# Optimization experiments

Hardware: AMD Instinct MI355X
Metric: run time of the kernel (lower is better)

The kernel has to match this reference:

```python
import jax, jax.numpy as jnp
import numpy as np

B, T, C, H = 2, 2048, 1024, 16
D = C // H  # head dim 64


def setup_inputs() -> dict:
    key = jax.random.key(0)
    k1, k2, k3, k4, k5 = jax.random.split(key, 5)
    s = 0.02
    return {
        "x": jax.random.normal(k1, (B, T, C), jnp.float32),
        "w_attn": jax.random.normal(k2, (C, 3 * C), jnp.float32) * s,
        "b_attn": jnp.zeros((3 * C,), jnp.float32),
        "w_proj": jax.random.normal(k3, (C, C), jnp.float32) * s,
        "b_proj": jnp.zeros((C,), jnp.float32),
    }


def reference(x, w_attn, b_attn, w_proj, b_proj):
    b, t, c = x.shape
    qkv = x @ w_attn + b_attn  # [B,T,3C]
    q, k, v = jnp.split(qkv, 3, axis=-1)
    # [B,T,C] -> [B,H,T,D]
    q = q.reshape(b, t, H, D).transpose(0, 2, 1, 3)
    k = k.reshape(b, t, H, D).transpose(0, 2, 1, 3)
    v = v.reshape(b, t, H, D).transpose(0, 2, 1, 3)
    scores = jnp.einsum("bhqd,bhkd->bhqk", q, k) * (1.0 / jnp.sqrt(jnp.float32(D)))
    causal = jnp.tril(jnp.ones((t, t), bool))
    scores = jnp.where(causal[None, None], scores, jnp.float32(-jnp.inf))
    attn = jax.nn.softmax(scores, axis=-1)
    out = jnp.einsum("bhqk,bhkd->bhqd", attn, v)  # [B,H,T,D]
    out = out.transpose(0, 2, 1, 3).reshape(b, t, c)
    return out @ w_proj + b_proj
```

## Files before the change

kernel.cpp:

```cpp
#include <hip/hip_runtime.h>
#include <hip/hip_bf16.h>

#define B_ 2
#define T_ 2048
#define C_ 1024
#define H_ 16
#define D_ 64
#define M1 4096
#define N1 3072
#define K_ 1024

typedef __attribute__((ext_vector_type(8))) __bf16 bf16x8;
typedef __attribute__((ext_vector_type(4))) float f32x4;
typedef __attribute__((ext_vector_type(8))) unsigned short ushort8_t;
typedef __attribute__((ext_vector_type(4))) unsigned short ushort4_t;
typedef __attribute__((ext_vector_type(2))) unsigned int uint2_t;

static __device__ __forceinline__ unsigned short f2bf(float f) {
    unsigned int u = __builtin_bit_cast(unsigned int, f);
    u += 0x7fffu + ((u >> 16) & 1u);
    return (unsigned short)(u >> 16);
}
static __device__ __forceinline__ unsigned short f2bf_hw(float f) {
    return __builtin_bit_cast(unsigned short, (__bf16)f);
}
static __device__ __forceinline__ unsigned int packbf(float lo, float hi) {
    return (unsigned int)f2bf_hw(lo) | ((unsigned int)f2bf_hw(hi) << 16);
}
static __device__ __forceinline__ bf16x8 bload(const unsigned short* p) {
    return __builtin_bit_cast(bf16x8, *(const ushort8_t*)p);
}

#if defined(__has_builtin)
#if __has_builtin(__builtin_amdgcn_exp2f)
#define HAVE_EXP2_BUILTIN 1
#endif
#endif
static __device__ __forceinline__ float fexp2(float x) {
#ifdef HAVE_EXP2_BUILTIN
    return __builtin_amdgcn_exp2f(x);
#else
    float r; asm("v_exp_f32 %0, %1" : "=v"(r) : "v"(x)); return r;
#endif
}

typedef __attribute__((address_space(1))) const unsigned int gu32;
typedef __attribute__((address_space(3))) unsigned int lu32;
static __device__ __forceinline__ void gld16(const void* g, void* l) {
    __builtin_amdgcn_global_load_lds((gu32*)g, (lu32*)l, 16, 0, 0);
}

#define VMCNT(n) asm volatile("s_waitcnt vmcnt(" #n ")" ::: "memory")
#define LGKM0    asm volatile("s_waitcnt lgkmcnt(0)" ::: "memory")

__global__ void cast_x_kernel(const float* __restrict__ in,
                              unsigned short* __restrict__ out, int n4) {
    int idx = blockIdx.x * blockDim.x + threadIdx.x;
    int stride = gridDim.x * blockDim.x;
    for (int i = idx; i < n4; i += stride) {
        float4 v = ((const float4*)in)[i];
        ushort4_t o;
        o.x = f2bf(v.x); o.y = f2bf(v.y); o.z = f2bf(v.z); o.w = f2bf(v.w);
        ((ushort4_t*)out)[i] = o;
    }
}

__global__ void transpose_cast_kernel(const float* __restrict__ in,
                                      unsigned short* __restrict__ out,
                                      int K, int N) {
    __shared__ float tile[32][33];
    int tx = threadIdx.x & 31;
    int ty = threadIdx.x >> 5;
    int n0 = blockIdx.x * 32;
    int k0 = blockIdx.y * 32;
#pragma unroll
    for (int rr = 0; rr < 32; rr += 8)
        tile[ty + rr][tx] = in[(size_t)(k0 + ty + rr) * N + n0 + tx];
    __syncthreads();
#pragma unroll
    for (int rr = 0; rr < 32; rr += 8)
        out[(size_t)(n0 + ty + rr) * K + k0 + tx] = f2bf(tile[tx][ty + rr]);
}

template <bool SWAP>
static __device__ __forceinline__ void gemm_loop(
    const unsigned short* __restrict__ A, const unsigned short* __restrict__ Bt,
    unsigned short (*As)[128 * 32], unsigned short (*Bs)[128 * 32],
    int row0, int col0, int tid, f32x4 (&acc)[4][4])
{
    const int lane = tid & 63;
    const int wave = tid >> 6;
    const int g = lane >> 4, cl = lane & 15;
    const int wr = (wave >> 1) * 64, wc = (wave & 1) * 64;
    const int srow = tid >> 2;
    const int sgran = tid & 3;
#pragma unroll
    for (int m = 0; m < 4; ++m)
#pragma unroll
        for (int n = 0; n < 4; ++n)
            acc[m][n] = (f32x4){0.f, 0.f, 0.f, 0.f};
    auto stage = [&](int buf, int k0) {
#pragma unroll
        for (int c = 0; c < 2; ++c) {
            int r = srow + c * 64;
            int lg = sgran ^ ((r >> 1) & 3);
            gld16(A + (size_t)(row0 + r) * K_ + k0 + lg * 8,
                  (char*)&As[buf][0] + c * 4096 + wave * 1024);
            gld16(Bt + (size_t)(col0 + r) * K_ + k0 + lg * 8,
                  (char*)&Bs[buf][0] + c * 4096 + wave * 1024);
        }
    };
    stage(0, 0);
    int buf = 0;
    for (int k0 = 0; k0 < K_; k0 += 32) {
        if (k0 + 32 < K_) { stage(buf ^ 1, k0 + 32); VMCNT(4); }
        else              { VMCNT(0); }
        __builtin_amdgcn_s_barrier();
        bf16x8 af[4], bfv[4];
#pragma unroll
        for (int m = 0; m < 4; ++m) {
            int ra = wr + m * 16 + cl;
            af[m] = bload(&As[buf][ra * 32 + (g ^ ((ra >> 1) & 3)) * 8]);
        }
#pragma unroll
        for (int n = 0; n < 4; ++n) {
            int rb = wc + n * 16 + cl;
            bfv[n] = bload(&Bs[buf][rb * 32 + (g ^ ((rb >> 1) & 3)) * 8]);
        }
#pragma unroll
        for (int m = 0; m < 4; ++m)
#pragma unroll
            for (int n = 0; n < 4; ++n)
                acc[m][n] = SWAP
                    ? __builtin_amdgcn_mfma_f32_16x16x32_bf16(bfv[n], af[m], acc[m][n], 0, 0, 0)
                    : __builtin_amdgcn_mfma_f32_16x16x32_bf16(af[m], bfv[n], acc[m][n], 0, 0, 0);
        LGKM0;
        __builtin_amdgcn_s_barrier();
        buf ^= 1;
    }
}

__global__ __launch_bounds__(256)
void gemm_qkv_kernel(const unsigned short* __restrict__ A,
                     const unsigned short* __restrict__ Bt,
                     const float* __restrict__ bias,
                     unsigned short* __restrict__ Qo,
                     unsigned short* __restrict__ Ko,
                     unsigned short* __restrict__ Vt)
{
    __shared__ unsigned short As[2][128 * 32];
    __shared__ unsigned short Bs[2][128 * 32];
    const int lin = blockIdx.x + gridDim.x * blockIdx.y;
    const int xcd = lin & 7;
    const int idx = lin >> 3;
    const int bx = (xcd >> 1) * 8 + (idx & 7);
    const int by = (xcd & 1) * 12 + (idx >> 3);
    const int row0 = bx * 128, col0 = by * 128;

    const int tid = threadIdx.x;
    const int lane = tid & 63;
    const int wave = tid >> 6;
    const int g = lane >> 4, cl = lane & 15;
    const int wr = (wave >> 1) * 64, wc = (wave & 1) * 64;
    const float QSCALE = 0.125f * 1.44269504088896340736f;

    f32x4 acc[4][4];
    if (by >= 16) {
        gemm_loop<false>(A, Bt, As, Bs, row0, col0, tid, acc);
#pragma unroll
        for (int m = 0; m < 4; ++m) {
            int i0 = row0 + wr + m * 16 + g * 4;
            int b = i0 >> 11, t0 = i0 & 2047;
#pragma unroll
            for (int n = 0; n < 4; ++n) {
                int j = col0 + wc + n * 16 + cl;
                int c = j & 1023;
                int h = c >> 6, d = c & 63;
                float bv = bias[j];
                size_t bh = (size_t)(b * H_ + h);
                uint2_t w;
                w.x = packbf(acc[m][n][0] + bv, acc[m][n][1] + bv);
                w.y = packbf(acc[m][n][2] + bv, acc[m][n][3] + bv);
                *(uint2_t*)&Vt[(bh * D_ + d) * T_ + t0] = w;
            }
        }
    } else {
        gemm_loop<true>(A, Bt, As, Bs, row0, col0, tid, acc);
        const int jbase = col0 + wc;
        const int which = jbase >> 10;
        const int h = (jbase & 1023) >> 6;
        unsigned short* dst = which ? Ko : Qo;
        const float s = which ? 1.0f : QSCALE;
#pragma unroll
        for (int m = 0; m < 4; ++m) {
            int i = row0 + wr + m * 16 + cl;
            int b = i >> 11, t = i & 2047;
            size_t bh = (size_t)(b * H_ + h);
#pragma unroll
            for (int n = 0; n < 4; ++n) {
                int d0 = n * 16 + g * 4;
                float4 bv = *(const float4*)&bias[jbase + d0];
                uint2_t w;
                w.x = packbf((acc[m][n][0] + bv.x) * s, (acc[m][n][1] + bv.y) * s);
                w.y = packbf((acc[m][n][2] + bv.z) * s, (acc[m][n][3] + bv.w) * s);
                *(uint2_t*)&dst[(bh * T_ + t) * D_ + d0] = w;
            }
        }
    }
}

__global__ __launch_bounds__(256)
void gemm_proj_kernel(const unsigned short* __restrict__ A,
                      const unsigned short* __restrict__ Bt,
                      const float* __restrict__ bias,
                      float* __restrict__ out)
{
    __shared__ unsigned short As[2][128 * 32];
    __shared__ unsigned short Bs[2][128 * 32];
    const int row0 = blockIdx.x * 128, col0 = blockIdx.y * 128;
    const int tid = threadIdx.x;
    const int lane = tid & 63;
    const int wave = tid >> 6;
    const int g = lane >> 4, cl = lane & 15;
    const int wr = (wave >> 1) * 64, wc = (wave & 1) * 64;

    f32x4 acc[4][4];
    gemm_loop<true>(A, Bt, As, Bs, row0, col0, tid, acc);

#pragma unroll
    for (int m = 0; m < 4; ++m) {
        int i = row0 + wr + m * 16 + cl;
#pragma unroll
        for (int n = 0; n < 4; ++n) {
            int j0 = col0 + wc + n * 16 + g * 4;
            float4 bv = *(const float4*)&bias[j0];
            f32x4 o = acc[m][n];
            o[0] += bv.x; o[1] += bv.y; o[2] += bv.z; o[3] += bv.w;
            *(f32x4*)&out[(size_t)i * C_ + j0] = o;
        }
    }
}

__global__ __launch_bounds__(256)
void attn_kernel(const unsigned short* __restrict__ Q,
                 const unsigned short* __restrict__ Kb,
                 const unsigned short* __restrict__ Vh_,
                 unsigned short* __restrict__ AO)
{
    __shared__ unsigned short Klds[2][64 * 64];
    __shared__ unsigned short Vlds[2][64 * 64];
    __shared__ unsigned short Plds[4][16 * 64];
    const int lin = blockIdx.x;
    const int idx = lin >> 3;
    const int bh  = (lin & 7) + 8 * (idx & 3);
    const int qt  = 31 - (idx >> 2);
    const int b = bh >> 4, h = bh & 15;
    const int tid = threadIdx.x;
    const int lane = tid & 63;
    const int wave = tid >> 6;
    const int g = lane >> 4, cl = lane & 15;

    const unsigned short* Qh = Q + (size_t)bh * T_ * D_;
    const unsigned short* Kh = Kb + (size_t)bh * T_ * D_;
    const unsigned short* Vh = Vh_ + (size_t)bh * D_ * T_;

    const int srow = tid >> 3;
    const int sg   = tid & 7;
    const int pswz = (cl & 7) << 4;

    auto stage = [&](int bufi, int kb) {
#pragma unroll
        for (int c = 0; c < 2; ++c) {
            int r = srow + c * 32;
            int lg = sg ^ (r & 7);
            gld16(Kh + (size_t)(kb + r) * D_ + lg * 8,
                  (char*)&Klds[bufi][0] + c * 4096 + wave * 1024);
            gld16(Vh + (size_t)r * T_ + kb + lg * 8,
                  (char*)&Vlds[bufi][0] + c * 4096 + wave * 1024);
        }
    };

    const int q0 = qt * 64 + wave * 16;
    const int tq = q0 + cl;

    bf16x8 qf[2];
#pragma unroll
    for (int c2 = 0; c2 < 2; ++c2)
        qf[c2] = bload(Qh + (size_t)(q0 + cl) * D_ + c2 * 32 + g * 8);

    f32x4 oacc[4];
#pragma unroll
    for (int n = 0; n < 4; ++n) oacc[n] = (f32x4){0.f, 0.f, 0.f, 0.f};
    float m_run = -INFINITY;
    float l_part = 0.f;

    const int nk = qt + 1;
    stage(0, 0);
    int buf = 0;
    for (int kt = 0; kt < nk; ++kt) {
        if (kt + 1 < nk) { stage(buf ^ 1, (kt + 1) * 64); VMCNT(4); }
        else             { VMCNT(0); }
        __builtin_amdgcn_s_barrier();

        const int kb = kt * 64;
        f32x4 sc[4];
        __builtin_amdgcn_s_setprio(1);
#pragma unroll
        for (int n = 0; n < 4; ++n) {
            sc[n] = (f32x4){0.f, 0.f, 0.f, 0.f};
#pragma unroll
            for (int c2 = 0; c2 < 2; ++c2) {
                int pg = (c2 * 4 + g) ^ (cl & 7);
                bf16x8 kf = bload(&Klds[buf][(n * 16 + cl) * 64 + pg * 8]);
                sc[n] = __builtin_amdgcn_mfma_f32_16x16x32_bf16(kf, qf[c2], sc[n], 0, 0, 0);
            }
        }
        __builtin_amdgcn_s_setprio(0);
        if (kt == qt) {
#pragma unroll
            for (int n = 0; n < 4; ++n) {
                int k4 = kb + n * 16 + g * 4;
#pragma unroll
                for (int r = 0; r < 4; ++r)
                    if (k4 + r > tq) sc[n][r] = -INFINITY;
            }
        }
        float mx[4];
#pragma unroll
        for (int n = 0; n < 4; ++n)
            mx[n] = fmaxf(fmaxf(sc[n][0], sc[n][1]), fmaxf(sc[n][2], sc[n][3]));
        float lm = fmaxf(fmaxf(mx[0], mx[1]), fmaxf(mx[2], mx[3]));
        if (!__all(lm <= m_run + 8.f)) {
            float vmax = lm;
            vmax = fmaxf(vmax, __shfl_xor(vmax, 16, 64));
            vmax = fmaxf(vmax, __shfl_xor(vmax, 32, 64));
            float mn = fmaxf(m_run, vmax);
            float alpha = fexp2(m_run - mn);
            l_part *= alpha;
#pragma unroll
            for (int n = 0; n < 4; ++n)
#pragma unroll
                for (int r = 0; r < 4; ++r) oacc[n][r] *= alpha;
            m_run = mn;
        }
        float p[4][4], psub[4];
#pragma unroll
        for (int n = 0; n < 4; ++n) {
#pragma unroll
            for (int r = 0; r < 4; ++r) p[n][r] = fexp2(sc[n][r] - m_run);
            psub[n] = (p[n][0] + p[n][1]) + (p[n][2] + p[n][3]);
        }
        l_part += (psub[0] + psub[1]) + (psub[2] + psub[3]);
#pragma unroll
        for (int n = 0; n < 4; ++n) {
            uint2_t w;
            w.x = packbf(p[n][0], p[n][1]);
            w.y = packbf(p[n][2], p[n][3]);
            *(uint2_t*)((char*)&Plds[wave][0] + ((cl * 128 + n * 32 + g * 8) ^ pswz)) = w;
        }
        bf16x8 pf[2];
#pragma unroll
        for (int kk = 0; kk < 2; ++kk)
            pf[kk] = bload((const unsigned short*)
                ((char*)&Plds[wave][0] + ((cl * 128 + kk * 64 + g * 16) ^ pswz)));
        __builtin_amdgcn_s_setprio(1);
#pragma unroll
        for (int n = 0; n < 4; ++n) {
#pragma unroll
            for (int kk = 0; kk < 2; ++kk) {
                int pg = (kk * 4 + g) ^ (cl & 7);
                bf16x8 vfr = bload(&Vlds[buf][(n * 16 + cl) * 64 + pg * 8]);
                oacc[n] = __builtin_amdgcn_mfma_f32_16x16x32_bf16(vfr, pf[kk], oacc[n], 0, 0, 0);
            }
        }
        __builtin_amdgcn_s_setprio(0);
        LGKM0;
        __builtin_amdgcn_s_barrier();
        buf ^= 1;
    }
    float lt = l_part;
    lt += __shfl_xor(lt, 16, 64);
    lt += __shfl_xor(lt, 32, 64);
    float inv = 1.f / lt;
#pragma unroll
    for (int n = 0; n < 4; ++n) {
        uint2_t w;
        w.x = packbf(oacc[n][0] * inv, oacc[n][1] * inv);
        w.y = packbf(oacc[n][2] * inv, oacc[n][3] * inv);
        *(uint2_t*)&AO[((size_t)b * T_ + tq) * C_ + h * D_ + n * 16 + g * 4] = w;
    }
}

extern "C" void kernel_launch(void* const* d_in, const int* in_sizes, int n_in,
                              void* d_out, int out_size, void* d_ws, size_t ws_size,
                              hipStream_t stream) {
    (void)in_sizes; (void)n_in; (void)out_size; (void)ws_size;
    const float* x      = (const float*)d_in[0];
    const float* w_attn = (const float*)d_in[1];
    const float* b_attn = (const float*)d_in[2];
    const float* w_proj = (const float*)d_in[3];
    const float* b_proj = (const float*)d_in[4];
    float* out = (float*)d_out;

    char* ws = (char*)d_ws;
    unsigned short* Xb  = (unsigned short*)(ws);
    unsigned short* Wt1 = (unsigned short*)(ws + ((size_t)8  << 20));
    unsigned short* Wt2 = (unsigned short*)(ws + ((size_t)14 << 20));
    unsigned short* Qb  = (unsigned short*)(ws + ((size_t)16 << 20));
    unsigned short* Kb  = (unsigned short*)(ws + ((size_t)24 << 20));
    unsigned short* Vt  = (unsigned short*)(ws + ((size_t)32 << 20));
    unsigned short* AO  = Xb;

    cast_x_kernel<<<1024, 256, 0, stream>>>(x, Xb, (M1 * K_) / 4);
    transpose_cast_kernel<<<dim3(N1 / 32, K_ / 32), 256, 0, stream>>>(w_attn, Wt1, K_, N1);
    transpose_cast_kernel<<<dim3(C_ / 32, K_ / 32), 256, 0, stream>>>(w_proj, Wt2, K_, C_);
    gemm_qkv_kernel<<<dim3(M1 / 128, N1 / 128), 256, 0, stream>>>(Xb, Wt1, b_attn, Qb, Kb, Vt);
    attn_kernel<<<1024, 256, 0, stream>>>(Qb, Kb, Vt, AO);
    gemm_proj_kernel<<<dim3(M1 / 128, C_ / 128), 256, 0, stream>>>(AO, Wt2, b_proj, out);
}
```

Before: 129.4 us.

## Use 8-wave 512-thread blocks for QKV and projection GEMMs

Both GEMM kernels move from 4 waves per 128x128 tile to 8 waves, each wave computing a 32x64 sub-tile with half the accumulators. Each thread now issues one staging load per operand per k-step. The QKV epilogue is unified to the non-swapped MFMA layout, so Q and K are written as scattered 2-byte stores instead of packed vector stores. The aim is more waves in flight to hide latency, at the cost of less register reuse per wave and uncoalesced Q/K writes.

```diff
diff --git a/kernel.cpp b/kernel.cpp
--- a/kernel.cpp
+++ b/kernel.cpp
@@ -83,42 +83,38 @@
 }
 
 template <bool SWAP>
-static __device__ __forceinline__ void gemm_loop(
+static __device__ __forceinline__ void gemm_loop8(
     const unsigned short* __restrict__ A, const unsigned short* __restrict__ Bt,
     unsigned short (*As)[128 * 32], unsigned short (*Bs)[128 * 32],
-    int row0, int col0, int tid, f32x4 (&acc)[4][4])
+    int row0, int col0, int tid, f32x4 (&acc)[2][4])
 {
     const int lane = tid & 63;
     const int wave = tid >> 6;
     const int g = lane >> 4, cl = lane & 15;
-    const int wr = (wave >> 1) * 64, wc = (wave & 1) * 64;
+    const int wr = (wave & 3) * 32, wc = (wave >> 2) * 64;
     const int srow = tid >> 2;
     const int sgran = tid & 3;
 #pragma unroll
-    for (int m = 0; m < 4; ++m)
+    for (int m = 0; m < 2; ++m)
 #pragma unroll
         for (int n = 0; n < 4; ++n)
             acc[m][n] = (f32x4){0.f, 0.f, 0.f, 0.f};
+    const int lg = sgran ^ ((srow >> 1) & 3);
     auto stage = [&](int buf, int k0) {
-#pragma unroll
-        for (int c = 0; c < 2; ++c) {
-            int r = srow + c * 64;
-            int lg = sgran ^ ((r >> 1) & 3);
-            gld16(A + (size_t)(row0 + r) * K_ + k0 + lg * 8,
-                  (char*)&As[buf][0] + c * 4096 + wave * 1024);
-            gld16(Bt + (size_t)(col0 + r) * K_ + k0 + lg * 8,
-                  (char*)&Bs[buf][0] + c * 4096 + wave * 1024);
-        }
+        gld16(A + (size_t)(row0 + srow) * K_ + k0 + lg * 8,
+              (char*)&As[buf][0] + wave * 1024);
+        gld16(Bt + (size_t)(col0 + srow) * K_ + k0 + lg * 8,
+              (char*)&Bs[buf][0] + wave * 1024);
     };
     stage(0, 0);
     int buf = 0;
     for (int k0 = 0; k0 < K_; k0 += 32) {
-        if (k0 + 32 < K_) { stage(buf ^ 1, k0 + 32); VMCNT(4); }
+        if (k0 + 32 < K_) { stage(buf ^ 1, k0 + 32); VMCNT(2); }
         else              { VMCNT(0); }
         __builtin_amdgcn_s_barrier();
-        bf16x8 af[4], bfv[4];
-#pragma unroll
-        for (int m = 0; m < 4; ++m) {
+        bf16x8 af[2], bfv[4];
+#pragma unroll
+        for (int m = 0; m < 2; ++m) {
             int ra = wr + m * 16 + cl;
             af[m] = bload(&As[buf][ra * 32 + (g ^ ((ra >> 1) & 3)) * 8]);
         }
@@ -128,7 +124,7 @@
             bfv[n] = bload(&Bs[buf][rb * 32 + (g ^ ((rb >> 1) & 3)) * 8]);
         }
 #pragma unroll
-        for (int m = 0; m < 4; ++m)
+        for (int m = 0; m < 2; ++m)
 #pragma unroll
             for (int n = 0; n < 4; ++n)
                 acc[m][n] = SWAP
@@ -140,7 +136,7 @@
     }
 }
 
-__global__ __launch_bounds__(256)
+__global__ __launch_bounds__(512, 4)
 void gemm_qkv_kernel(const unsigned short* __restrict__ A,
                      const unsigned short* __restrict__ Bt,
                      const float* __restrict__ bias,
@@ -161,55 +157,49 @@
     const int lane = tid & 63;
     const int wave = tid >> 6;
     const int g = lane >> 4, cl = lane & 15;
-    const int wr = (wave >> 1) * 64, wc = (wave & 1) * 64;
+    const int wr = (wave & 3) * 32, wc = (wave >> 2) * 64;
+
+    f32x4 acc[2][4];
+    gemm_loop8<false>(A, Bt, As, Bs, row0, col0, tid, acc);
+
     const float QSCALE = 0.125f * 1.44269504088896340736f;
-
-    f32x4 acc[4][4];
-    if (by >= 16) {
-        gemm_loop<false>(A, Bt, As, Bs, row0, col0, tid, acc);
-#pragma unroll
-        for (int m = 0; m < 4; ++m) {
-            int i0 = row0 + wr + m * 16 + g * 4;
-            int b = i0 >> 11, t0 = i0 & 2047;
-#pragma unroll
-            for (int n = 0; n < 4; ++n) {
-                int j = col0 + wc + n * 16 + cl;
-                int c = j & 1023;
-                int h = c >> 6, d = c & 63;
-                float bv = bias[j];
-                size_t bh = (size_t)(b * H_ + h);
+#pragma unroll
+    for (int m = 0; m < 2; ++m) {
+        int i0 = row0 + wr + m * 16 + g * 4;
+        int b = i0 >> 11, t0 = i0 & 2047;
+#pragma unroll
+        for (int n = 0; n < 4; ++n) {
+            int j = col0 + wc + n * 16 + cl;
+            int which = j >> 10;
+            int c = j & 1023;
+            int h = c >> 6, d = c & 63;
+            float bv = bias[j];
+            size_t bh = (size_t)(b * H_ + h);
+            float v0 = acc[m][n][0] + bv;
+            float v1 = acc[m][n][1] + bv;
+            float v2 = acc[m][n][2] + bv;
+            float v3 = acc[m][n][3] + bv;
+            if (which == 2) {
                 uint2_t w;
-                w.x = packbf(acc[m][n][0] + bv, acc[m][n][1] + bv);
-                w.y = packbf(acc[m][n][2] + bv, acc[m][n][3] + bv);
+                w.x = packbf(v0, v1);
+                w.y = packbf(v2, v3);
                 *(uint2_t*)&Vt[(bh * D_ + d) * T_ + t0] = w;
+            } else if (which == 0) {
+                Qo[(bh * T_ + t0 + 0) * D_ + d] = f2bf_hw(v0 * QSCALE);
+                Qo[(bh * T_ + t0 + 1) * D_ + d] = f2bf_hw(v1 * QSCALE);
+                Qo[(bh * T_ + t0 + 2) * D_ + d] = f2bf_hw(v2 * QSCALE);
+                Qo[(bh * T_ + t0 + 3) * D_ + d] = f2bf_hw(v3 * QSCALE);
+            } else {
+                Ko[(bh * T_ + t0 + 0) * D_ + d] = f2bf_hw(v0);
+                Ko[(bh * T_ + t0 + 1) * D_ + d] = f2bf_hw(v1);
+                Ko[(bh * T_ + t0 + 2) * D_ + d] = f2bf_hw(v2);
+                Ko[(bh * T_ + t0 + 3) * D_ + d] = f2bf_hw(v3);
             }
         }
-    } else {
-        gemm_loop<true>(A, Bt, As, Bs, row0, col0, tid, acc);
-        const int jbase = col0 + wc;
-        const int which = jbase >> 10;
-        const int h = (jbase & 1023) >> 6;
-        unsigned short* dst = which ? Ko : Qo;
-        const float s = which ? 1.0f : QSCALE;
-#pragma unroll
-        for (int m = 0; m < 4; ++m) {
-            int i = row0 + wr + m * 16 + cl;
-            int b = i >> 11, t = i & 2047;
-            size_t bh = (size_t)(b * H_ + h);
-#pragma unroll
-            for (int n = 0; n < 4; ++n) {
-                int d0 = n * 16 + g * 4;
-                float4 bv = *(const float4*)&bias[jbase + d0];
-                uint2_t w;
-                w.x = packbf((acc[m][n][0] + bv.x) * s, (acc[m][n][1] + bv.y) * s);
-                w.y = packbf((acc[m][n][2] + bv.z) * s, (acc[m][n][3] + bv.w) * s);
-                *(uint2_t*)&dst[(bh * T_ + t) * D_ + d0] = w;
-            }
-        }
-    }
-}
-
-__global__ __launch_bounds__(256)
+    }
+}
+
+__global__ __launch_bounds__(512, 4)
 void gemm_proj_kernel(const unsigned short* __restrict__ A,
                       const unsigned short* __restrict__ Bt,
                       const float* __restrict__ bias,
@@ -222,13 +212,13 @@
     const int lane = tid & 63;
     const int wave = tid >> 6;
     const int g = lane >> 4, cl = lane & 15;
-    const int wr = (wave >> 1) * 64, wc = (wave & 1) * 64;
-
-    f32x4 acc[4][4];
-    gemm_loop<true>(A, Bt, As, Bs, row0, col0, tid, acc);
-
-#pragma unroll
-    for (int m = 0; m < 4; ++m) {
+    const int wr = (wave & 3) * 32, wc = (wave >> 2) * 64;
+
+    f32x4 acc[2][4];
+    gemm_loop8<true>(A, Bt, As, Bs, row0, col0, tid, acc);
+
+#pragma unroll
+    for (int m = 0; m < 2; ++m) {
         int i = row0 + wr + m * 16 + cl;
 #pragma unroll
         for (int n = 0; n < 4; ++n) {
@@ -414,7 +404,7 @@
     cast_x_kernel<<<1024, 256, 0, stream>>>(x, Xb, (M1 * K_) / 4);
     transpose_cast_kernel<<<dim3(N1 / 32, K_ / 32), 256, 0, stream>>>(w_attn, Wt1, K_, N1);
     transpose_cast_kernel<<<dim3(C_ / 32, K_ / 32), 256, 0, stream>>>(w_proj, Wt2, K_, C_);
-    gemm_qkv_kernel<<<dim3(M1 / 128, N1 / 128), 256, 0, stream>>>(Xb, Wt1, b_attn, Qb, Kb, Vt);
+    gemm_qkv_kernel<<<dim3(M1 / 128, N1 / 128), 512, 0, stream>>>(Xb, Wt1, b_attn, Qb, Kb, Vt);
     attn_kernel<<<1024, 256, 0, stream>>>(Qb, Kb, Vt, AO);
-    gemm_proj_kernel<<<dim3(M1 / 128, C_ / 128), 256, 0, stream>>>(AO, Wt2, b_proj, out);
-}
+    gemm_proj_kernel<<<dim3(M1 / 128, C_ / 128), 512, 0, stream>>>(AO, Wt2, b_proj, out);
+}
```

Measured after the change: 114.5 us. -11.5%, faster.
